# Kernel optimization log

Measured on AMD Instinct MI355X. Metric: run time of the kernel, lower is better.

## Reference

```python
import jax, jax.numpy as jnp
import numpy as np

H = 512        # hidden_size
E = 512        # embedding_size
VOCAB = 32
OPS = 16
B = 64         # batch of trees
N = 1023       # complete binary tree, depth 9 (2^10 - 1 nodes)
TEMP = 3.0
INT_TYPES_MAX = 1  # types 0 (INT_PO) and 1 (INT_NE) carry a numeric arg


def setup_inputs() -> dict:
    key = jax.random.key(0)
    ks = jax.random.split(key, 12)
    s = 0.05
    return {
        "node_types": jax.random.randint(ks[0], (B, N), 0, VOCAB),
        "node_args": jax.random.normal(ks[1], (B, N), jnp.float32),
        "validity_mask": jax.random.uniform(ks[2], (B, OPS), jnp.float32, 1e-3, 1.0),
        "emb_table": jax.random.normal(ks[3], (VOCAB, E), jnp.float32) * s,
        "W_ih": jax.random.normal(ks[4], (8 * H, E), jnp.float32) * s,
        "W_hh": jax.random.normal(ks[5], (8 * H, 2 * H), jnp.float32) * s,
        "b_ih": jax.random.normal(ks[6], (8 * H,), jnp.float32) * s,
        "b_hh": jax.random.normal(ks[7], (8 * H,), jnp.float32) * s,
        "W1": jax.random.normal(ks[8], (H, H), jnp.float32) * s,
        "b1": jax.random.normal(ks[9], (H,), jnp.float32) * s,
        "W2": jax.random.normal(ks[10], (OPS, H), jnp.float32) * s,
        "b2": jax.random.normal(ks[11], (OPS,), jnp.float32) * s,
    }


def reference(node_types, node_args, validity_mask, emb_table,
              W_ih, W_hh, b_ih, b_hh, W1, b1, W2, b2):
    # --- SympleEmbedding: per-node embedding; int-typed nodes carry arg in last slot
    emb = emb_table[node_types]                                   # [B, N, E]
    is_int = node_types <= INT_TYPES_MAX                          # [B, N]
    emb = emb.at[..., -1].set(jnp.where(is_int, node_args, emb[..., -1]))

    # --- BinaryTreeLSTM, batched level-by-level (heap layout: children of i are 2i+1, 2i+2)
    D = int(np.log2(N + 1)) - 1                                   # depth of internal levels-1 = 9
    h = jnp.zeros((B, N, H), emb.dtype)                           # leaves: zeros
    c = jnp.zeros((B, N, H), emb.dtype)
    bias = b_ih + b_hh
    for d in range(D - 1, -1, -1):                                # bottom-up over internal levels
        idx = np.arange(2 ** d - 1, 2 ** (d + 1) - 1)             # nodes at level d
        left, right = 2 * idx + 1, 2 * idx + 2
        h0 = jnp.concatenate([h[:, left], h[:, right]], axis=-1)  # [B, n, 2H]
        c0 = jnp.concatenate([c[:, left], c[:, right]], axis=-1)
        gates = (jnp.einsum('bne,ge->bng', emb[:, idx], W_ih)
                 + jnp.einsum('bnh,gh->bng', h0, W_hh) + bias)    # [B, n, 8H]
        i_g, f_g, g_g, o_g = jnp.split(gates, 4, axis=-1)         # torch LSTM gate order i,f,g,o
        c_new = jax.nn.sigmoid(f_g) * c0 + jax.nn.sigmoid(i_g) * jnp.tanh(g_g)
        h_new = jax.nn.sigmoid(o_g) * jnp.tanh(c_new)
        h = h.at[:, idx].set(h_new[..., :H])                      # keep first H (as in module)
        c = c.at[:, idx].set(c_new[..., :H])

    # --- actor FFN on root hidden + validity-masked tempered softmax
    root_h = h[:, 0]                                              # [B, H]
    x = jax.nn.relu(root_h @ W1.T + b1)
    logits = x @ W2.T + b2 + jnp.log(validity_mask)
    return jax.nn.softmax(logits / TEMP, axis=-1)                 # [B, OPS]
```

## Files before the change

kernel.cpp:

```cpp
#include <hip/hip_runtime.h>
#include <hip/hip_cooperative_groups.h>
#include <math.h>

namespace cg = cooperative_groups;

#define Nn 1023

typedef __attribute__((ext_vector_type(8))) short short8;
typedef __attribute__((ext_vector_type(4))) float f32x4;

#define AS1(p) ((const __attribute__((address_space(1))) void*)(p))
#define AS3(p) ((__attribute__((address_space(3))) void*)(p))

__device__ __forceinline__ float sigf(float x) { return 1.0f / (1.0f + __expf(-x)); }
__device__ __forceinline__ float tanhfast(float x) {
    float e = __expf(2.0f * x);
    return 1.0f - 2.0f / (e + 1.0f);
}
__device__ __forceinline__ unsigned short f2bf(float x) {
    unsigned u = __float_as_uint(x);
    return (unsigned short)((u + 0x7fffu + ((u >> 16) & 1u)) >> 16);
}
__device__ __forceinline__ float bf2f(unsigned short b) {
    return __uint_as_float(((unsigned)b) << 16);
}

__global__ __launch_bounds__(256) void prep_all(
    const float* __restrict__ W_hh, unsigned short* __restrict__ WhT,
    const float* __restrict__ W1, float* __restrict__ W1t,
    const int* __restrict__ node_types, const float* __restrict__ node_args,
    const float* __restrict__ emb, const float* __restrict__ W2,
    float* __restrict__ W2t, int* __restrict__ tyv, float* __restrict__ alphaf,
    const float* __restrict__ W_ih, const float* __restrict__ b_ih,
    const float* __restrict__ b_hh, float* __restrict__ E32b,
    float* __restrict__ w511f, int* __restrict__ rowidx, int* __restrict__ cnt) {
    int bid = blockIdx.x, t = threadIdx.x;
    if (bid < 1024) {
        int idx = bid * 256 + t;
        int P = idx >> 7;
        int k0 = (idx & 127) * 8;
        int row = ((P >> 4) & 3) * 1024 + (P >> 6) * 16 + (P & 15);
        const float* src = W_hh + (size_t)row * 1024 + k0;
        float4 v0 = *(const float4*)src;
        float4 v1 = *(const float4*)(src + 4);
        short8 o;
        o[0] = (short)f2bf(v0.x); o[1] = (short)f2bf(v0.y);
        o[2] = (short)f2bf(v0.z); o[3] = (short)f2bf(v0.w);
        o[4] = (short)f2bf(v1.x); o[5] = (short)f2bf(v1.y);
        o[6] = (short)f2bf(v1.z); o[7] = (short)f2bf(v1.w);
        *(short8*)(WhT + (size_t)P * 1024 + k0) = o;
    } else if (bid < 1088) {
        __shared__ float tile[64][65];
        int idx2 = bid - 1024;
        int jb = (idx2 & 7) * 64, kb = (idx2 >> 3) * 64;
        #pragma unroll
        for (int i = 0; i < 16; ++i) {
            int idx = t + i * 256;
            int lj = idx >> 6, lk = idx & 63;
            tile[lj][lk] = W1[(jb + lj) * 512 + kb + lk];
        }
        __syncthreads();
        #pragma unroll
        for (int i = 0; i < 16; ++i) {
            int idx = t + i * 256;
            int lk = idx >> 6, lj = idx & 63;
            W1t[(kb + lk) * 512 + jb + lj] = tile[lj][lk];
        }
    } else if (bid < 1216) {
        int gid = (bid - 1088) * 256 + t;
        if (gid < 32704) {
            int node = gid >> 6, b = gid & 63;
            int ty = node_types[b * Nn + node];
            tyv[gid] = ty;
            alphaf[gid] = (ty <= 1) ? (node_args[b * Nn + node] - emb[ty * 512 + 511]) : 0.f;
        }
        if (gid < 8192) {
            int k = gid >> 4, op = gid & 15;
            W2t[gid] = W2[op * 512 + k];
        }
    } else if (bid < 1472) {
        int o = (bid - 1216) * 256 + t;
        int ty = o >> 11, P = o & 2047;
        int row = ((P >> 4) & 3) * 1024 + (P >> 6) * 16 + (P & 15);
        const float* er = emb + (size_t)ty * 512;
        const float* wr = W_ih + (size_t)row * 512;
        float s = b_ih[row] + b_hh[row];
        for (int k = 0; k < 512; k += 4) {
            float4 e4 = *(const float4*)(er + k);
            float4 w4 = *(const float4*)(wr + k);
            s = fmaf(e4.x, w4.x, fmaf(e4.y, w4.y, fmaf(e4.z, w4.z, fmaf(e4.w, w4.w, s))));
        }
        E32b[o] = s;
        if (ty == 0) w511f[P] = wr[511];
    } else {
        int z = (bid - 1472) * 256 + t;
        if (z < 8448) rowidx[z] = 0;
        if (bid == 1472 && t == 0) *cnt = 0;
    }
}

__global__ __launch_bounds__(256) void leaf_tables(
    const float* __restrict__ E32b,
    unsigned short* __restrict__ Hleaf, float* __restrict__ Hleaf_f,
    float* __restrict__ Cleaf) {
    int o = blockIdx.x * 256 + threadIdx.x;
    int ty = o >> 9, j = o & 511;
    int Pb = (j >> 4) * 64 + (j & 15);
    const float* Er = E32b + (size_t)ty * 2048;
    float ig = Er[Pb], gg = Er[Pb + 32], og = Er[Pb + 48];
    float cn = sigf(ig) * tanhfast(gg);
    float hn = sigf(og) * tanhfast(cn);
    Hleaf[o] = f2bf(hn);
    Hleaf_f[o] = hn;
    Cleaf[o] = cn;
}

__global__ __launch_bounds__(256) void leaf_side(
    const float* __restrict__ E32b, const float* __restrict__ w511f,
    const int* __restrict__ tyv, const float* __restrict__ alphaf,
    unsigned short* __restrict__ Hside, float* __restrict__ Cside,
    const float* __restrict__ W_hh, const float* __restrict__ Hleaf_f,
    float* __restrict__ GLt, float* __restrict__ GRt,
    int* __restrict__ rowidx, int* __restrict__ cnt) {
    int bid = blockIdx.x, t = threadIdx.x;
    if (bid < 4096) {
        int r = bid * 4 + (t >> 6);
        int gn = 16320 + r;
        int ty = tyv[gn];
        if (ty > 1) return;
        float al = alphaf[gn];
        int l = r >> 6, b = r & 63;
        int jc = (t & 63) * 8;
        const float* Er = E32b + (size_t)ty * 2048;
        short8 hv;
        float cv[8];
        #pragma unroll
        for (int jj = 0; jj < 8; ++jj) {
            int j = jc + jj;
            int Pb = (j >> 4) * 64 + (j & 15);
            float ig = Er[Pb]      + al * w511f[Pb];
            float gg = Er[Pb + 32] + al * w511f[Pb + 32];
            float og = Er[Pb + 48] + al * w511f[Pb + 48];
            float cn = sigf(ig) * tanhfast(gg);
            float hn = sigf(og) * tanhfast(cn);
            hv[jj] = (short)f2bf(hn);
            cv[jj] = cn;
        }
        *(short8*)(Hside + (size_t)r * 512 + jc) = hv;
        if ((l & 1) == 0) {
            size_t cr = ((size_t)((l >> 1) * 64 + b)) * 512 + jc;
            float4 c0 = {cv[0], cv[1], cv[2], cv[3]};
            float4 c1 = {cv[4], cv[5], cv[6], cv[7]};
            *(float4*)(Cside + cr) = c0;
            *(float4*)(Cside + cr + 4) = c1;
        }
    } else if (bid < 4608) {
        int gid = (bid - 4096) * 256 + t;
        int side = gid >> 16, ty = (gid >> 11) & 31, P = gid & 2047;
        int row = ((P >> 4) & 3) * 1024 + (P >> 6) * 16 + (P & 15);
        const float* wr = W_hh + (size_t)row * 1024 + side * 512;
        const float* hr = Hleaf_f + (size_t)ty * 512;
        float s = 0.f;
        for (int k = 0; k < 512; k += 4) {
            float4 w4 = *(const float4*)(wr + k);
            float4 h4 = *(const float4*)(hr + k);
            s = fmaf(w4.x, h4.x, fmaf(w4.y, h4.y, fmaf(w4.z, h4.z, fmaf(w4.w, h4.w, s))));
        }
        if (side == 0) GLt[ty * 2048 + P] = s;
        else           GRt[ty * 2048 + P] = s;
    } else {
        int r = (bid - 4608) * 256 + t;
        int lf = (r >> 6) * 128 + (r & 63);
        if (tyv[16320 + lf] <= 1 || tyv[16320 + lf + 64] <= 1) {
            int p = atomicAdd(cnt, 1);
            rowidx[p] = r;
        }
    }
}

__global__ void zero_out(float* __restrict__ outp, int n) {
    int i = blockIdx.x * 256 + threadIdx.x;
    if (i < n) outp[i] = 0.f;
}

__device__ __forceinline__ void d7_table_body(
    char* smemraw,
    const float* __restrict__ E32b, const float* __restrict__ GLt,
    const float* __restrict__ GRt, const float* __restrict__ Cleaf,
    const float* __restrict__ Cside, const float* __restrict__ w511f,
    const int* __restrict__ tyv, const float* __restrict__ alphaf,
    unsigned short* __restrict__ out_h, float* __restrict__ out_c,
    int bx, int by) {
    float* Es  = (float*)smemraw;
    float* GLs = Es + 32 * 129;
    float* GRs = GLs + 32 * 129;
    float* Cls = GRs + 32 * 129;
    float* w5s = Cls + 32 * 33;
    const int t = threadIdx.x;
    const int j0 = by * 32;
    const int r = bx * 256 + t;

    for (int i = t; i < 32 * 128; i += 256) {
        int ty = i >> 7, pp = i & 127;
        int gp = ((j0 >> 4) + (pp >> 6)) * 64 + (pp & 63);
        Es[ty * 129 + pp]  = E32b[ty * 2048 + gp];
        GLs[ty * 129 + pp] = GLt[ty * 2048 + gp];
        GRs[ty * 129 + pp] = GRt[ty * 2048 + gp];
    }
    for (int i = t; i < 32 * 32; i += 256) {
        int ty = i >> 5, jl = i & 31;
        Cls[ty * 33 + jl] = Cleaf[ty * 512 + j0 + jl];
    }
    if (t < 128) w5s[t] = w511f[((j0 >> 4) + (t >> 6)) * 64 + (t & 63)];
    __syncthreads();

    int gn = 8128 + r;
    int tyP = tyv[gn];
    float aP = alphaf[gn];
    int lf = (r >> 6) * 128 + (r & 63);
    int tyL = tyv[16320 + lf];
    int tyR = tyv[16320 + lf + 64];
    bool intL = (tyL <= 1);
    bool evenl = (((r >> 6) & 1) == 0);
    size_t crow = ((size_t)((r >> 7) * 64 + (r & 63))) * 512;

    #pragma unroll
    for (int j8 = 0; j8 < 4; ++j8) {
        short8 hv;
        float cv[8];
        #pragma unroll
        for (int jj = 0; jj < 8; ++jj) {
            int jl = j8 * 8 + jj;
            int ppb = (jl >> 4) * 64 + (jl & 15);
            float ig = Es[tyP * 129 + ppb]      + aP * w5s[ppb]      + GLs[tyL * 129 + ppb]      + GRs[tyR * 129 + ppb];
            float fg = Es[tyP * 129 + ppb + 16] + aP * w5s[ppb + 16] + GLs[tyL * 129 + ppb + 16] + GRs[tyR * 129 + ppb + 16];
            float gg = Es[tyP * 129 + ppb + 32] + aP * w5s[ppb + 32] + GLs[tyL * 129 + ppb + 32] + GRs[tyR * 129 + ppb + 32];
            float og = Es[tyP * 129 + ppb + 48] + aP * w5s[ppb + 48] + GLs[tyL * 129 + ppb + 48] + GRs[tyR * 129 + ppb + 48];
            float cl = intL ? Cside[(size_t)r * 512 + j0 + jl] : Cls[tyL * 33 + jl];
            float cn = sigf(fg) * cl + sigf(ig) * tanhfast(gg);
            float hn = sigf(og) * tanhfast(cn);
            hv[jj] = (short)f2bf(hn);
            cv[jj] = cn;
        }
        *(short8*)(out_h + (size_t)r * 512 + j0 + j8 * 8) = hv;
        if (evenl) {
            float4 c0 = {cv[0], cv[1], cv[2], cv[3]};
            float4 c1 = {cv[4], cv[5], cv[6], cv[7]};
            *(float4*)(out_c + crow + j0 + j8 * 8) = c0;
            *(float4*)(out_c + crow + j0 + j8 * 8 + 4) = c1;
        }
    }
    __syncthreads();
}

template<int MODE>
__device__ __forceinline__ void mfma_tile(
    char* smemraw,
    const unsigned short* __restrict__ WhT, const float* __restrict__ E32b,
    const float* __restrict__ w511f,
    const int* __restrict__ tyv, const float* __restrict__ alphaf,
    const unsigned short* __restrict__ in_h, const float* __restrict__ in_c,
    const unsigned short* __restrict__ Hleaf, const unsigned short* __restrict__ Hside,
    const float* __restrict__ Cleaf, const float* __restrict__ Cside,
    const int* __restrict__ rowidx,
    unsigned short* __restrict__ out_h, float* __restrict__ out_c,
    int base, int nloc, int bx, int by) {
    unsigned short* AB = (unsigned short*)smemraw;
    const int t = threadIdx.x;
    const int w = t >> 6, lane = t & 63;
    const int wr = w >> 1, wc = w & 1;
    const int lane15 = lane & 15, lg = lane >> 4;
    const int M = nloc * 64;
    const int brow0 = bx * 128;
    const int bcol0 = by * 128;
    const int lanek8 = (lane & 7) * 8;

    const unsigned short* baseL[4];
    const unsigned short* baseR[4];
    const unsigned short* wB[4];
    #pragma unroll
    for (int q = 0; q < 4; ++q) {
        int m = w * 32 + q * 8 + (lane >> 3);
        int r = brow0 + m;
        if (MODE == 2) r = rowidx[r];
        else if (r > M - 1) r = M - 1;
        int lf = (r >> 6) * 128 + (r & 63);
        if (MODE >= 1) {
            int tyL = tyv[16320 + lf];
            int tyR = tyv[16320 + lf + 64];
            baseL[q] = (tyL <= 1) ? (Hside + (size_t)lf * 512)
                                  : (Hleaf + (size_t)tyL * 512);
            baseR[q] = (tyR <= 1) ? (Hside + (size_t)(lf + 64) * 512)
                                  : (Hleaf + (size_t)tyR * 512);
        } else {
            baseL[q] = in_h + (size_t)lf * 512;
            baseR[q] = baseL[q] + 64 * 512;
        }
        int P = bcol0 + w * 32 + q * 8 + (lane >> 3);
        wB[q] = WhT + (size_t)P * 1024;
    }

    auto stage = [&](int kt, int cur) {
        unsigned short* Ad = AB + cur * 16384;
        unsigned short* Bd = Ad + 8192;
        #pragma unroll
        for (int q = 0; q < 4; ++q) {
            const unsigned short* s = (kt < 8) ? (baseL[q] + kt * 64)
                                               : (baseR[q] + (kt - 8) * 64);
            __builtin_amdgcn_global_load_lds(AS1(s + lanek8),
                                             AS3(Ad + w * 2048 + q * 512), 16, 0, 0);
            __builtin_amdgcn_global_load_lds(AS1(wB[q] + kt * 64 + lanek8),
                                             AS3(Bd + w * 2048 + q * 512), 16, 0, 0);
        }
    };

    stage(0, 0);

    f32x4 acc[4][4];
    float w4[4];
    int P4[4];
    int rr[4][4];
    #pragma unroll
    for (int q = 0; q < 4; ++q) {
        P4[q] = bcol0 + wc * 64 + q * 16 + lane15;
        w4[q] = w511f[P4[q]];
    }
    #pragma unroll
    for (int mi = 0; mi < 4; ++mi) {
        #pragma unroll
        for (int reg = 0; reg < 4; ++reg) {
            int r = brow0 + wr * 64 + mi * 16 + lg * 4 + reg;
            if (MODE == 2) r = rowidx[r];
            else if (r > M - 1) r = M - 1;
            rr[mi][reg] = r;
            int gn = base * 64 + r;
            int ty = tyv[gn];
            float al = alphaf[gn];
            const float* Er = E32b + (size_t)ty * 2048;
            #pragma unroll
            for (int q = 0; q < 4; ++q)
                acc[mi][q][reg] = Er[P4[q]] + al * w4[q];
        }
    }

    int cur = 0;
    for (int kt = 0; kt < 16; ++kt) {
        __syncthreads();
        if (kt < 15) stage(kt + 1, cur ^ 1);
        const unsigned short* Ac = AB + cur * 16384;
        const unsigned short* Bc = Ac + 8192;
        #pragma unroll
        for (int ks = 0; ks < 2; ++ks) {
            short8 av[4], bv[4];
            #pragma unroll
            for (int mi = 0; mi < 4; ++mi)
                av[mi] = *(const short8*)(Ac + (wr * 64 + mi * 16 + lane15) * 64 + ks * 32 + lg * 8);
            #pragma unroll
            for (int q = 0; q < 4; ++q)
                bv[q] = *(const short8*)(Bc + (wc * 64 + q * 16 + lane15) * 64 + ks * 32 + lg * 8);
            #pragma unroll
            for (int mi = 0; mi < 4; ++mi)
                #pragma unroll
                for (int q = 0; q < 4; ++q)
                    acc[mi][q] = __builtin_amdgcn_mfma_f32_16x16x32_bf16(av[mi], bv[q], acc[mi][q], 0, 0, 0);
        }
        cur ^= 1;
    }

    const int j = (by * 2 + wc) * 16 + lane15;
    #pragma unroll
    for (int mi = 0; mi < 4; ++mi) {
        #pragma unroll
        for (int reg = 0; reg < 4; ++reg) {
            int r = rr[mi][reg];
            if (r < M) {
                float ig = acc[mi][0][reg];
                float fg = acc[mi][1][reg];
                float gg = acc[mi][2][reg];
                float og = acc[mi][3][reg];
                float cl;
                if (MODE >= 1) {
                    int lf = (r >> 6) * 128 + (r & 63);
                    int tyL = tyv[16320 + lf];
                    cl = (tyL <= 1) ? Cside[(size_t)r * 512 + j]
                                    : Cleaf[(size_t)tyL * 512 + j];
                } else {
                    cl = in_c[(size_t)r * 512 + j];
                }
                float cn = sigf(fg) * cl + sigf(ig) * tanhfast(gg);
                float hn = sigf(og) * tanhfast(cn);
                out_h[(size_t)r * 512 + j] = f2bf(hn);
                if (((r >> 6) & 1) == 0)
                    out_c[((size_t)((r >> 7) * 64 + (r & 63))) * 512 + j] = cn;
            }
        }
    }
}

__device__ __forceinline__ void head_body(
    char* smemraw,
    const unsigned short* __restrict__ rootH, const float* __restrict__ W1t,
    const float* __restrict__ b1, const float* __restrict__ W2t,
    const float* __restrict__ b2, const float* __restrict__ vmask,
    float* __restrict__ outp, int b) {
    float* rh = (float*)smemraw;
    float* xs = rh + 512;
    float* part = xs + 512;
    int t = threadIdx.x;
    rh[t] = bf2f(rootH[b * 512 + t]);
    rh[t + 256] = bf2f(rootH[b * 512 + t + 256]);
    __syncthreads();
    #pragma unroll
    for (int jj = 0; jj < 2; ++jj) {
        int jx = t + jj * 256;
        float acc = b1[jx];
        for (int k = 0; k < 512; ++k) acc = fmaf(rh[k], W1t[k * 512 + jx], acc);
        xs[jx] = fmaxf(acc, 0.f);
    }
    __syncthreads();
    int op = t & 15, seg = t >> 4;
    float p = 0.f;
    for (int k = seg * 32; k < seg * 32 + 32; ++k) p = fmaf(xs[k], W2t[k * 16 + op], p);
    part[seg * 17 + op] = p;
    __syncthreads();
    if (t < 16) {
        float s = 0.f;
        #pragma unroll
        for (int g = 0; g < 16; ++g) s += part[g * 17 + t];
        float logit = s + b2[t] + logf(vmask[b * 16 + t]);
        float z = logit * (1.0f / 3.0f);
        float m = z;
        for (int o2 = 8; o2; o2 >>= 1) m = fmaxf(m, __shfl_xor(m, o2, 16));
        float e = __expf(z - m);
        float ssum = e;
        for (int o2 = 8; o2; o2 >>= 1) ssum += __shfl_xor(ssum, o2, 16);
        outp[b * 16 + t] = e / ssum;
    }
}

__global__ __launch_bounds__(256) void tree_main(
    const unsigned short* WhT, const float* E32b, const float* w511f,
    const int* tyv, const float* alphaf,
    const unsigned short* Hleaf, const unsigned short* Hside,
    const float* Cleaf, const float* Cside,
    const float* GLt, const float* GRt,
    const int* rowidx, const int* cnt,
    unsigned short* Xh, float* Xc, unsigned short* Yh, float* Yc,
    const float* W1t, const float* b1, const float* W2t, const float* b2,
    const float* vmask, float* outp) {
    cg::grid_group grid = cg::this_grid();
    extern __shared__ char smem[];
    const int bid = blockIdx.x;

    d7_table_body(smem, E32b, GLt, GRt, Cleaf, Cside, w511f, tyv, alphaf,
                  Xh, Xc, bid & 31, bid >> 5);
    __threadfence(); grid.sync();

    {
        int nc = *cnt;
        int rb = ((nc + 127) & ~127) >> 7;
        int ntiles = rb * 16;
        for (int T = bid; T < ntiles; T += 512)
            mfma_tile<2>(smem, WhT, E32b, w511f, tyv, alphaf, nullptr, nullptr,
                         Hleaf, Hside, Cleaf, Cside, rowidx,
                         Xh, Xc, 127, 128, T % rb, T / rb);
    }
    __threadfence(); grid.sync();

    for (int d = 6; d >= 0; --d) {
        int nloc = 1 << d;
        int gx = (nloc >= 2) ? (nloc >> 1) : 1;
        unsigned short* oh = (d & 1) ? Xh : Yh;
        float* oc          = (d & 1) ? Xc : Yc;
        const unsigned short* ih = (d & 1) ? Yh : Xh;
        const float* ic          = (d & 1) ? Yc : Xc;
        int ntiles = gx * 16;
        if (bid < ntiles)
            mfma_tile<0>(smem, WhT, E32b, w511f, tyv, alphaf, ih, ic,
                         nullptr, nullptr, nullptr, nullptr, nullptr,
                         oh, oc, nloc - 1, nloc, bid % gx, bid / gx);
        __threadfence(); grid.sync();
    }

    if (bid < 64)
        head_body(smem, Yh, W1t, b1, W2t, b2, vmask, outp, bid);
}

__global__ __launch_bounds__(256) void d7_table_cell_k(
    const float* __restrict__ E32b, const float* __restrict__ GLt,
    const float* __restrict__ GRt, const float* __restrict__ Cleaf,
    const float* __restrict__ Cside, const float* __restrict__ w511f,
    const int* __restrict__ tyv, const float* __restrict__ alphaf,
    unsigned short* __restrict__ out_h, float* __restrict__ out_c) {
    extern __shared__ char smem[];
    d7_table_body(smem, E32b, GLt, GRt, Cleaf, Cside, w511f, tyv, alphaf,
                  out_h, out_c, blockIdx.x, blockIdx.y);
}

template<int MODE>
__global__ __launch_bounds__(256) void lstm_mfma_k(
    const unsigned short* __restrict__ WhT, const float* __restrict__ E32b,
    const float* __restrict__ w511f,
    const int* __restrict__ tyv, const float* __restrict__ alphaf,
    const unsigned short* __restrict__ in_h, const float* __restrict__ in_c,
    const unsigned short* __restrict__ Hleaf, const unsigned short* __restrict__ Hside,
    const float* __restrict__ Cleaf, const float* __restrict__ Cside,
    const int* __restrict__ rowidx, const int* __restrict__ cnt,
    unsigned short* __restrict__ out_h, float* __restrict__ out_c,
    int base, int nloc) {
    extern __shared__ char smem[];
    if (MODE == 2) {
        int nc = *cnt;
        int padded = (nc + 127) & ~127;
        if ((int)blockIdx.x * 128 >= padded) return;
    }
    mfma_tile<MODE>(smem, WhT, E32b, w511f, tyv, alphaf, in_h, in_c,
                    Hleaf, Hside, Cleaf, Cside, rowidx,
                    out_h, out_c, base, nloc, blockIdx.x, blockIdx.y);
}

__global__ __launch_bounds__(256) void head_k(
    const unsigned short* __restrict__ rootH, const float* __restrict__ W1t,
    const float* __restrict__ b1, const float* __restrict__ W2t,
    const float* __restrict__ b2, const float* __restrict__ vmask,
    float* __restrict__ outp) {
    extern __shared__ char smem[];
    head_body(smem, rootH, W1t, b1, W2t, b2, vmask, outp, blockIdx.x);
}

extern "C" void kernel_launch(void* const* d_in, const int* in_sizes, int n_in,
                              void* d_out, int out_size, void* d_ws, size_t ws_size,
                              hipStream_t stream) {
    const int*   node_types = (const int*)d_in[0];
    const float* node_args  = (const float*)d_in[1];
    const float* vmask      = (const float*)d_in[2];
    const float* emb_table  = (const float*)d_in[3];
    const float* W_ih       = (const float*)d_in[4];
    const float* W_hh       = (const float*)d_in[5];
    const float* b_ih       = (const float*)d_in[6];
    const float* b_hh       = (const float*)d_in[7];
    const float* W1         = (const float*)d_in[8];
    const float* b1         = (const float*)d_in[9];
    const float* W2         = (const float*)d_in[10];
    const float* b2         = (const float*)d_in[11];
    float* out = (float*)d_out;

    char* ws = (char*)d_ws;
    size_t off = 0;
    auto alloc = [&](size_t bytes) { char* p = ws + off; off += (bytes + 255) & ~(size_t)255; return p; };
    unsigned short* WhT  = (unsigned short*)alloc((size_t)2048 * 1024 * 2);
    float* E32b          = (float*)alloc((size_t)32 * 2048 * 4);
    float* w511f         = (float*)alloc(2048 * 4);
    float* W1t           = (float*)alloc((size_t)512 * 512 * 4);
    float* W2t           = (float*)alloc(8192 * 4);
    int*   tyv           = (int*)alloc(32704 * 4);
    float* alphaf        = (float*)alloc(32704 * 4);
    unsigned short* Hleaf= (unsigned short*)alloc((size_t)32 * 512 * 2);
    float* Hleaf_f       = (float*)alloc((size_t)32 * 512 * 4);
    float* Cleaf         = (float*)alloc((size_t)32 * 512 * 4);
    float* GLt           = (float*)alloc((size_t)32 * 2048 * 4);
    float* GRt           = (float*)alloc((size_t)32 * 2048 * 4);
    int*   rowidx        = (int*)alloc(8448 * 4);
    int*   cnt           = (int*)alloc(256);
    unsigned short* Hside= (unsigned short*)alloc((size_t)16384 * 512 * 2);
    float* Cside         = (float*)alloc((size_t)8192 * 512 * 4);
    unsigned short* Xh   = (unsigned short*)alloc((size_t)8192 * 512 * 2);
    unsigned short* Yh   = (unsigned short*)alloc((size_t)4096 * 512 * 2);
    float* Xc            = (float*)alloc((size_t)4096 * 512 * 4);
    float* Yc            = (float*)alloc((size_t)2048 * 512 * 4);

    if (ws_size < off) {
        zero_out<<<(out_size + 255) / 256, 256, 0, stream>>>(out, out_size);
        return;
    }

    prep_all<<<1505, 256, 0, stream>>>(W_hh, WhT, W1, W1t, node_types, node_args,
                                       emb_table, W2, W2t, tyv, alphaf,
                                       W_ih, b_ih, b_hh, E32b, w511f, rowidx, cnt);
    leaf_tables<<<64, 256, 0, stream>>>(E32b, Hleaf, Hleaf_f, Cleaf);
    leaf_side<<<4640, 256, 0, stream>>>(E32b, w511f, tyv, alphaf, Hside, Cside,
                                        W_hh, Hleaf_f, GLt, GRt, rowidx, cnt);

    bool coop_ok = false;
    {
        int occ = 0;
        hipError_t qe = hipOccupancyMaxActiveBlocksPerMultiprocessor(
            &occ, tree_main, 256, 65536);
        if (qe == hipSuccess && occ >= 2) coop_ok = true;
    }
    if (coop_ok) {
        const unsigned short* cWhT = WhT;  const float* cE32b = E32b;
        const float* cw511 = w511f;        const int* ctyv = tyv;
        const float* calpha = alphaf;      const unsigned short* cHleaf = Hleaf;
        const unsigned short* cHside = Hside; const float* cCleaf = Cleaf;
        const float* cCside = Cside;       const float* cGL = GLt;
        const float* cGR = GRt;            const int* cridx = rowidx;
        const int* ccnt = cnt;             const float* cW1t = W1t;
        const float* cW2t = W2t;
        void* kargs[] = {
            (void*)&cWhT, (void*)&cE32b, (void*)&cw511, (void*)&ctyv, (void*)&calpha,
            (void*)&cHleaf, (void*)&cHside, (void*)&cCleaf, (void*)&cCside,
            (void*)&cGL, (void*)&cGR, (void*)&cridx, (void*)&ccnt,
            (void*)&Xh, (void*)&Xc, (void*)&Yh, (void*)&Yc,
            (void*)&cW1t, (void*)&b1, (void*)&cW2t, (void*)&b2,
            (void*)&vmask, (void*)&out };
        hipError_t le = hipLaunchCooperativeKernel(
            tree_main, dim3(512), dim3(256), kargs, (unsigned)65536, stream);
        if (le != hipSuccess) coop_ok = false;
    }
    if (!coop_ok) {
        d7_table_cell_k<<<dim3(32, 16), 256, 54272, stream>>>(
            E32b, GLt, GRt, Cleaf, Cside, w511f, tyv, alphaf, Xh, Xc);
        lstm_mfma_k<2><<<dim3(64, 16), 256, 65536, stream>>>(
            WhT, E32b, w511f, tyv, alphaf, nullptr, nullptr,
            Hleaf, Hside, Cleaf, Cside, rowidx, cnt, Xh, Xc, 127, 128);
        for (int d = 6; d >= 0; --d) {
            int nloc = 1 << d;
            unsigned short* oh = (d & 1) ? Xh : Yh;
            float* oc          = (d & 1) ? Xc : Yc;
            const unsigned short* ih = (d & 1) ? Yh : Xh;
            const float* ic          = (d & 1) ? Yc : Xc;
            int gx = (nloc >= 2) ? (nloc / 2) : 1;
            lstm_mfma_k<0><<<dim3(gx, 16), 256, 65536, stream>>>(
                WhT, E32b, w511f, tyv, alphaf, ih, ic,
                nullptr, nullptr, nullptr, nullptr,
                nullptr, nullptr, oh, oc, nloc - 1, nloc);
        }
        head_k<<<64, 256, 5184, stream>>>(Yh, W1t, b1, W2t, b2, vmask, out);
    }
}
```

Before: 448.8 us.

## Fold leaf-side setup and GL/GR table GEMM into cooperative tree kernel

Removes the separate leaf_tables and leaf_side launches and moves leaf computation, side-leaf state and the row-index compaction into a phase inside the cooperative tree kernel. The GL/GR child-contribution tables are now computed with a bf16 MFMA GEMM over a block-diagonal leaf matrix instead of scalar fp32 dot products. d7 table rows with any int-typed child are skipped because the compacted MFMA pass covers them, and the E32b dot product gets four accumulators. This cuts launch overhead and scalar work at the cost of an extra grid sync and bf16 rounding in the GL/GR tables.

```diff
diff --git a/kernel.cpp b/kernel.cpp
--- a/kernel.cpp
+++ b/kernel.cpp
@@ -84,13 +84,22 @@
         int row = ((P >> 4) & 3) * 1024 + (P >> 6) * 16 + (P & 15);
         const float* er = emb + (size_t)ty * 512;
         const float* wr = W_ih + (size_t)row * 512;
-        float s = b_ih[row] + b_hh[row];
-        for (int k = 0; k < 512; k += 4) {
-            float4 e4 = *(const float4*)(er + k);
-            float4 w4 = *(const float4*)(wr + k);
-            s = fmaf(e4.x, w4.x, fmaf(e4.y, w4.y, fmaf(e4.z, w4.z, fmaf(e4.w, w4.w, s))));
-        }
-        E32b[o] = s;
+        float s0 = b_ih[row] + b_hh[row], s1 = 0.f, s2 = 0.f, s3 = 0.f;
+        for (int k = 0; k < 512; k += 16) {
+            float4 e0 = *(const float4*)(er + k);
+            float4 w0 = *(const float4*)(wr + k);
+            float4 e1 = *(const float4*)(er + k + 4);
+            float4 w1 = *(const float4*)(wr + k + 4);
+            float4 e2 = *(const float4*)(er + k + 8);
+            float4 w2 = *(const float4*)(wr + k + 8);
+            float4 e3 = *(const float4*)(er + k + 12);
+            float4 w3 = *(const float4*)(wr + k + 12);
+            s0 = fmaf(e0.x, w0.x, fmaf(e0.y, w0.y, fmaf(e0.z, w0.z, fmaf(e0.w, w0.w, s0))));
+            s1 = fmaf(e1.x, w1.x, fmaf(e1.y, w1.y, fmaf(e1.z, w1.z, fmaf(e1.w, w1.w, s1))));
+            s2 = fmaf(e2.x, w2.x, fmaf(e2.y, w2.y, fmaf(e2.z, w2.z, fmaf(e2.w, w2.w, s2))));
+            s3 = fmaf(e3.x, w3.x, fmaf(e3.y, w3.y, fmaf(e3.z, w3.z, fmaf(e3.w, w3.w, s3))));
+        }
+        E32b[o] = (s0 + s1) + (s2 + s3);
         if (ty == 0) w511f[P] = wr[511];
     } else {
         int z = (bid - 1472) * 256 + t;
@@ -99,77 +108,76 @@
     }
 }
 
-__global__ __launch_bounds__(256) void leaf_tables(
-    const float* __restrict__ E32b,
-    unsigned short* __restrict__ Hleaf, float* __restrict__ Hleaf_f,
-    float* __restrict__ Cleaf) {
-    int o = blockIdx.x * 256 + threadIdx.x;
-    int ty = o >> 9, j = o & 511;
-    int Pb = (j >> 4) * 64 + (j & 15);
-    const float* Er = E32b + (size_t)ty * 2048;
-    float ig = Er[Pb], gg = Er[Pb + 32], og = Er[Pb + 48];
-    float cn = sigf(ig) * tanhfast(gg);
-    float hn = sigf(og) * tanhfast(cn);
-    Hleaf[o] = f2bf(hn);
-    Hleaf_f[o] = hn;
-    Cleaf[o] = cn;
-}
-
-__global__ __launch_bounds__(256) void leaf_side(
+__global__ void zero_out(float* __restrict__ outp, int n) {
+    int i = blockIdx.x * 256 + threadIdx.x;
+    if (i < n) outp[i] = 0.f;
+}
+
+__device__ __forceinline__ void ph0_body(
+    int bid,
     const float* __restrict__ E32b, const float* __restrict__ w511f,
     const int* __restrict__ tyv, const float* __restrict__ alphaf,
+    unsigned short* __restrict__ Hleaf, float* __restrict__ Cleaf,
+    unsigned short* __restrict__ A64,
     unsigned short* __restrict__ Hside, float* __restrict__ Cside,
-    const float* __restrict__ W_hh, const float* __restrict__ Hleaf_f,
-    float* __restrict__ GLt, float* __restrict__ GRt,
     int* __restrict__ rowidx, int* __restrict__ cnt) {
-    int bid = blockIdx.x, t = threadIdx.x;
-    if (bid < 4096) {
-        int r = bid * 4 + (t >> 6);
-        int gn = 16320 + r;
-        int ty = tyv[gn];
-        if (ty > 1) return;
-        float al = alphaf[gn];
-        int l = r >> 6, b = r & 63;
-        int jc = (t & 63) * 8;
+    const int t = threadIdx.x;
+    if (bid < 64) {
+        int o = bid * 256 + t;
+        int ty = o >> 9, j = o & 511;
+        int Pb = (j >> 4) * 64 + (j & 15);
         const float* Er = E32b + (size_t)ty * 2048;
-        short8 hv;
-        float cv[8];
-        #pragma unroll
-        for (int jj = 0; jj < 8; ++jj) {
-            int j = jc + jj;
-            int Pb = (j >> 4) * 64 + (j & 15);
-            float ig = Er[Pb]      + al * w511f[Pb];
-            float gg = Er[Pb + 32] + al * w511f[Pb + 32];
-            float og = Er[Pb + 48] + al * w511f[Pb + 48];
-            float cn = sigf(ig) * tanhfast(gg);
-            float hn = sigf(og) * tanhfast(cn);
-            hv[jj] = (short)f2bf(hn);
-            cv[jj] = cn;
-        }
-        *(short8*)(Hside + (size_t)r * 512 + jc) = hv;
-        if ((l & 1) == 0) {
-            size_t cr = ((size_t)((l >> 1) * 64 + b)) * 512 + jc;
-            float4 c0 = {cv[0], cv[1], cv[2], cv[3]};
-            float4 c1 = {cv[4], cv[5], cv[6], cv[7]};
-            *(float4*)(Cside + cr) = c0;
-            *(float4*)(Cside + cr + 4) = c1;
-        }
-    } else if (bid < 4608) {
-        int gid = (bid - 4096) * 256 + t;
-        int side = gid >> 16, ty = (gid >> 11) & 31, P = gid & 2047;
-        int row = ((P >> 4) & 3) * 1024 + (P >> 6) * 16 + (P & 15);
-        const float* wr = W_hh + (size_t)row * 1024 + side * 512;
-        const float* hr = Hleaf_f + (size_t)ty * 512;
-        float s = 0.f;
-        for (int k = 0; k < 512; k += 4) {
-            float4 w4 = *(const float4*)(wr + k);
-            float4 h4 = *(const float4*)(hr + k);
-            s = fmaf(w4.x, h4.x, fmaf(w4.y, h4.y, fmaf(w4.z, h4.z, fmaf(w4.w, h4.w, s))));
-        }
-        if (side == 0) GLt[ty * 2048 + P] = s;
-        else           GRt[ty * 2048 + P] = s;
-    } else {
-        int r = (bid - 4608) * 256 + t;
+        float ig = Er[Pb], gg = Er[Pb + 32], og = Er[Pb + 48];
+        float cn = sigf(ig) * tanhfast(gg);
+        float hn = sigf(og) * tanhfast(cn);
+        unsigned short hb = f2bf(hn);
+        Hleaf[o] = hb;
+        Cleaf[o] = cn;
+        A64[ty * 1024 + j] = hb;
+        A64[ty * 1024 + 512 + j] = 0;
+        A64[(32 + ty) * 1024 + j] = 0;
+        A64[(32 + ty) * 1024 + 512 + j] = hb;
+    }
+    {
+        int wave = t >> 6, jc = (t & 63) * 8;
+        int r0 = bid * 32 + wave * 8;
+        int tys[8];
+        #pragma unroll
+        for (int i = 0; i < 8; ++i) tys[i] = tyv[16320 + r0 + i];
+        #pragma unroll
+        for (int i = 0; i < 8; ++i) {
+            if (tys[i] > 1) continue;
+            int r = r0 + i;
+            int gn = 16320 + r;
+            float al = alphaf[gn];
+            int l = r >> 6, b = r & 63;
+            const float* Er = E32b + (size_t)tys[i] * 2048;
+            short8 hv;
+            float cv[8];
+            #pragma unroll
+            for (int jj = 0; jj < 8; ++jj) {
+                int j = jc + jj;
+                int Pb = (j >> 4) * 64 + (j & 15);
+                float ig = Er[Pb]      + al * w511f[Pb];
+                float gg = Er[Pb + 32] + al * w511f[Pb + 32];
+                float og = Er[Pb + 48] + al * w511f[Pb + 48];
+                float cn = sigf(ig) * tanhfast(gg);
+                float hn = sigf(og) * tanhfast(cn);
+                hv[jj] = (short)f2bf(hn);
+                cv[jj] = cn;
+            }
+            *(short8*)(Hside + (size_t)r * 512 + jc) = hv;
+            if ((l & 1) == 0) {
+                size_t cr = ((size_t)((l >> 1) * 64 + b)) * 512 + jc;
+                float4 c0 = {cv[0], cv[1], cv[2], cv[3]};
+                float4 c1 = {cv[4], cv[5], cv[6], cv[7]};
+                *(float4*)(Cside + cr) = c0;
+                *(float4*)(Cside + cr + 4) = c1;
+            }
+        }
+    }
+    if (bid >= 64 && bid < 96) {
+        int r = (bid - 64) * 256 + t;
         int lf = (r >> 6) * 128 + (r & 63);
         if (tyv[16320 + lf] <= 1 || tyv[16320 + lf + 64] <= 1) {
             int p = atomicAdd(cnt, 1);
@@ -178,16 +186,96 @@
     }
 }
 
-__global__ void zero_out(float* __restrict__ outp, int n) {
-    int i = blockIdx.x * 256 + threadIdx.x;
-    if (i < n) outp[i] = 0.f;
+template<int KT, bool BIAS>
+__device__ __forceinline__ void table_gemm_body(
+    char* smemraw, const unsigned short* __restrict__ Abf,
+    const unsigned short* __restrict__ Bt, const float* __restrict__ biasP,
+    float* __restrict__ C0, float* __restrict__ C1, int by) {
+    unsigned short* AB = (unsigned short*)smemraw;
+    const int t = threadIdx.x;
+    const int w = t >> 6, lane = t & 63;
+    const int wr = w >> 1, wc = w & 1;
+    const int lane15 = lane & 15, lg = lane >> 4;
+    const int bcol0 = by * 128;
+    const int lanek8 = (lane & 7) * 8;
+    const int ROWS = BIAS ? 32 : 64;
+
+    const unsigned short* aA[4];
+    const unsigned short* wB[4];
+    #pragma unroll
+    for (int q = 0; q < 4; ++q) {
+        int m = w * 32 + q * 8 + (lane >> 3);
+        int r = (m < ROWS) ? m : (ROWS - 1);
+        aA[q] = Abf + (size_t)r * (KT * 64);
+        int P = bcol0 + w * 32 + q * 8 + (lane >> 3);
+        wB[q] = Bt + (size_t)P * (KT * 64);
+    }
+    auto stage = [&](int kt, int cur) {
+        unsigned short* Ad = AB + cur * 16384;
+        unsigned short* Bd = Ad + 8192;
+        #pragma unroll
+        for (int q = 0; q < 4; ++q) {
+            __builtin_amdgcn_global_load_lds(AS1(aA[q] + kt * 64 + lanek8),
+                                             AS3(Ad + w * 2048 + q * 512), 16, 0, 0);
+            __builtin_amdgcn_global_load_lds(AS1(wB[q] + kt * 64 + lanek8),
+                                             AS3(Bd + w * 2048 + q * 512), 16, 0, 0);
+        }
+    };
+    stage(0, 0);
+    f32x4 acc[4][4];
+    int P4[4];
+    #pragma unroll
+    for (int q = 0; q < 4; ++q) P4[q] = bcol0 + wc * 64 + q * 16 + lane15;
+    #pragma unroll
+    for (int mi = 0; mi < 4; ++mi)
+        #pragma unroll
+        for (int reg = 0; reg < 4; ++reg)
+            #pragma unroll
+            for (int q = 0; q < 4; ++q)
+                acc[mi][q][reg] = BIAS ? biasP[P4[q]] : 0.f;
+    int cur = 0;
+    for (int kt = 0; kt < KT; ++kt) {
+        __syncthreads();
+        if (kt < KT - 1) stage(kt + 1, cur ^ 1);
+        const unsigned short* Ac = AB + cur * 16384;
+        const unsigned short* Bc = Ac + 8192;
+        #pragma unroll
+        for (int ks = 0; ks < 2; ++ks) {
+            short8 av[4], bv[4];
+            #pragma unroll
+            for (int mi = 0; mi < 4; ++mi)
+                av[mi] = *(const short8*)(Ac + (wr * 64 + mi * 16 + lane15) * 64 + ks * 32 + lg * 8);
+            #pragma unroll
+            for (int q = 0; q < 4; ++q)
+                bv[q] = *(const short8*)(Bc + (wc * 64 + q * 16 + lane15) * 64 + ks * 32 + lg * 8);
+            #pragma unroll
+            for (int mi = 0; mi < 4; ++mi)
+                #pragma unroll
+                for (int q = 0; q < 4; ++q)
+                    acc[mi][q] = __builtin_amdgcn_mfma_f32_16x16x32_bf16(av[mi], bv[q], acc[mi][q], 0, 0, 0);
+        }
+        cur ^= 1;
+    }
+    #pragma unroll
+    for (int mi = 0; mi < 4; ++mi)
+        #pragma unroll
+        for (int reg = 0; reg < 4; ++reg) {
+            int ro = wr * 64 + mi * 16 + lg * 4 + reg;
+            #pragma unroll
+            for (int q = 0; q < 4; ++q) {
+                float v = acc[mi][q][reg];
+                if (ro < 32) C0[(size_t)ro * 2048 + P4[q]] = v;
+                else if (!BIAS && ro < 64) C1[(size_t)(ro - 32) * 2048 + P4[q]] = v;
+            }
+        }
+    __syncthreads();
 }
 
 __device__ __forceinline__ void d7_table_body(
     char* smemraw,
     const float* __restrict__ E32b, const float* __restrict__ GLt,
     const float* __restrict__ GRt, const float* __restrict__ Cleaf,
-    const float* __restrict__ Cside, const float* __restrict__ w511f,
+    const float* __restrict__ w511f,
     const int* __restrict__ tyv, const float* __restrict__ alphaf,
     unsigned short* __restrict__ out_h, float* __restrict__ out_c,
     int bx, int by) {
@@ -220,34 +308,36 @@
     int lf = (r >> 6) * 128 + (r & 63);
     int tyL = tyv[16320 + lf];
     int tyR = tyv[16320 + lf + 64];
-    bool intL = (tyL <= 1);
+    bool skip = (tyL <= 1) || (tyR <= 1);
     bool evenl = (((r >> 6) & 1) == 0);
     size_t crow = ((size_t)((r >> 7) * 64 + (r & 63))) * 512;
 
-    #pragma unroll
-    for (int j8 = 0; j8 < 4; ++j8) {
-        short8 hv;
-        float cv[8];
-        #pragma unroll
-        for (int jj = 0; jj < 8; ++jj) {
-            int jl = j8 * 8 + jj;
-            int ppb = (jl >> 4) * 64 + (jl & 15);
-            float ig = Es[tyP * 129 + ppb]      + aP * w5s[ppb]      + GLs[tyL * 129 + ppb]      + GRs[tyR * 129 + ppb];
-            float fg = Es[tyP * 129 + ppb + 16] + aP * w5s[ppb + 16] + GLs[tyL * 129 + ppb + 16] + GRs[tyR * 129 + ppb + 16];
-            float gg = Es[tyP * 129 + ppb + 32] + aP * w5s[ppb + 32] + GLs[tyL * 129 + ppb + 32] + GRs[tyR * 129 + ppb + 32];
-            float og = Es[tyP * 129 + ppb + 48] + aP * w5s[ppb + 48] + GLs[tyL * 129 + ppb + 48] + GRs[tyR * 129 + ppb + 48];
-            float cl = intL ? Cside[(size_t)r * 512 + j0 + jl] : Cls[tyL * 33 + jl];
-            float cn = sigf(fg) * cl + sigf(ig) * tanhfast(gg);
-            float hn = sigf(og) * tanhfast(cn);
-            hv[jj] = (short)f2bf(hn);
-            cv[jj] = cn;
-        }
-        *(short8*)(out_h + (size_t)r * 512 + j0 + j8 * 8) = hv;
-        if (evenl) {
-            float4 c0 = {cv[0], cv[1], cv[2], cv[3]};
-            float4 c1 = {cv[4], cv[5], cv[6], cv[7]};
-            *(float4*)(out_c + crow + j0 + j8 * 8) = c0;
-            *(float4*)(out_c + crow + j0 + j8 * 8 + 4) = c1;
+    if (!skip) {
+        #pragma unroll
+        for (int j8 = 0; j8 < 4; ++j8) {
+            short8 hv;
+            float cv[8];
+            #pragma unroll
+            for (int jj = 0; jj < 8; ++jj) {
+                int jl = j8 * 8 + jj;
+                int ppb = (jl >> 4) * 64 + (jl & 15);
+                float ig = Es[tyP * 129 + ppb]      + aP * w5s[ppb]      + GLs[tyL * 129 + ppb]      + GRs[tyR * 129 + ppb];
+                float fg = Es[tyP * 129 + ppb + 16] + aP * w5s[ppb + 16] + GLs[tyL * 129 + ppb + 16] + GRs[tyR * 129 + ppb + 16];
+                float gg = Es[tyP * 129 + ppb + 32] + aP * w5s[ppb + 32] + GLs[tyL * 129 + ppb + 32] + GRs[tyR * 129 + ppb + 32];
+                float og = Es[tyP * 129 + ppb + 48] + aP * w5s[ppb + 48] + GLs[tyL * 129 + ppb + 48] + GRs[tyR * 129 + ppb + 48];
+                float cl = Cls[tyL * 33 + jl];
+                float cn = sigf(fg) * cl + sigf(ig) * tanhfast(gg);
+                float hn = sigf(og) * tanhfast(cn);
+                hv[jj] = (short)f2bf(hn);
+                cv[jj] = cn;
+            }
+            *(short8*)(out_h + (size_t)r * 512 + j0 + j8 * 8) = hv;
+            if (evenl) {
+                float4 c0 = {cv[0], cv[1], cv[2], cv[3]};
+                float4 c1 = {cv[4], cv[5], cv[6], cv[7]};
+                *(float4*)(out_c + crow + j0 + j8 * 8) = c0;
+                *(float4*)(out_c + crow + j0 + j8 * 8 + 4) = c1;
+            }
         }
     }
     __syncthreads();
@@ -262,7 +352,7 @@
     const unsigned short* __restrict__ in_h, const float* __restrict__ in_c,
     const unsigned short* __restrict__ Hleaf, const unsigned short* __restrict__ Hside,
     const float* __restrict__ Cleaf, const float* __restrict__ Cside,
-    const int* __restrict__ rowidx,
+    const int* __restrict__ rowidx, int nc,
     unsigned short* __restrict__ out_h, float* __restrict__ out_c,
     int base, int nloc, int bx, int by) {
     unsigned short* AB = (unsigned short*)smemraw;
@@ -281,11 +371,15 @@
     #pragma unroll
     for (int q = 0; q < 4; ++q) {
         int m = w * 32 + q * 8 + (lane >> 3);
-        int r = brow0 + m;
-        if (MODE == 2) r = rowidx[r];
-        else if (r > M - 1) r = M - 1;
+        int r;
+        if (MODE == 2) {
+            int idx = brow0 + m; if (idx > nc - 1) idx = nc - 1;
+            r = rowidx[idx];
+        } else {
+            r = brow0 + m; if (r > M - 1) r = M - 1;
+        }
         int lf = (r >> 6) * 128 + (r & 63);
-        if (MODE >= 1) {
+        if (MODE == 2) {
             int tyL = tyv[16320 + lf];
             int tyR = tyv[16320 + lf + 64];
             baseL[q] = (tyL <= 1) ? (Hside + (size_t)lf * 512)
@@ -329,9 +423,15 @@
     for (int mi = 0; mi < 4; ++mi) {
         #pragma unroll
         for (int reg = 0; reg < 4; ++reg) {
-            int r = brow0 + wr * 64 + mi * 16 + lg * 4 + reg;
-            if (MODE == 2) r = rowidx[r];
-            else if (r > M - 1) r = M - 1;
+            int r;
+            if (MODE == 2) {
+                int idx = brow0 + wr * 64 + mi * 16 + lg * 4 + reg;
+                if (idx > nc - 1) idx = nc - 1;
+                r = rowidx[idx];
+            } else {
+                r = brow0 + wr * 64 + mi * 16 + lg * 4 + reg;
+                if (r > M - 1) r = M - 1;
+            }
             rr[mi][reg] = r;
             int gn = base * 64 + r;
             int ty = tyv[gn];
@@ -379,7 +479,7 @@
                 float gg = acc[mi][2][reg];
                 float og = acc[mi][3][reg];
                 float cl;
-                if (MODE >= 1) {
+                if (MODE == 2) {
                     int lf = (r >> 6) * 128 + (r & 63);
                     int tyL = tyv[16320 + lf];
                     cl = (tyL <= 1) ? Cside[(size_t)r * 512 + j]
@@ -441,10 +541,9 @@
 __global__ __launch_bounds__(256) void tree_main(
     const unsigned short* WhT, const float* E32b, const float* w511f,
     const int* tyv, const float* alphaf,
-    const unsigned short* Hleaf, const unsigned short* Hside,
-    const float* Cleaf, const float* Cside,
-    const float* GLt, const float* GRt,
-    const int* rowidx, const int* cnt,
+    unsigned short* Hleaf, unsigned short* Hside,
+    float* Cleaf, float* Cside, unsigned short* A64,
+    float* GLt, float* GRt, int* rowidx, int* cnt,
     unsigned short* Xh, float* Xc, unsigned short* Yh, float* Yc,
     const float* W1t, const float* b1, const float* W2t, const float* b2,
     const float* vmask, float* outp) {
@@ -452,17 +551,22 @@
     extern __shared__ char smem[];
     const int bid = blockIdx.x;
 
-    d7_table_body(smem, E32b, GLt, GRt, Cleaf, Cside, w511f, tyv, alphaf,
+    ph0_body(bid, E32b, w511f, tyv, alphaf, Hleaf, Cleaf, A64, Hside, Cside,
+             rowidx, cnt);
+    __threadfence(); grid.sync();
+
+    if (bid < 16)
+        table_gemm_body<16, false>(smem, A64, WhT, nullptr, GLt, GRt, bid);
+    __threadfence(); grid.sync();
+
+    d7_table_body(smem, E32b, GLt, GRt, Cleaf, w511f, tyv, alphaf,
                   Xh, Xc, bid & 31, bid >> 5);
-    __threadfence(); grid.sync();
-
     {
         int nc = *cnt;
         int rb = ((nc + 127) & ~127) >> 7;
-        int ntiles = rb * 16;
-        for (int T = bid; T < ntiles; T += 512)
+        for (int T = bid; T < rb * 16; T += 512)
             mfma_tile<2>(smem, WhT, E32b, w511f, tyv, alphaf, nullptr, nullptr,
-                         Hleaf, Hside, Cleaf, Cside, rowidx,
+                         Hleaf, Hside, Cleaf, Cside, rowidx, nc,
                          Xh, Xc, 127, 128, T % rb, T / rb);
     }
     __threadfence(); grid.sync();
@@ -477,7 +581,7 @@
         int ntiles = gx * 16;
         if (bid < ntiles)
             mfma_tile<0>(smem, WhT, E32b, w511f, tyv, alphaf, ih, ic,
-                         nullptr, nullptr, nullptr, nullptr, nullptr,
+                         nullptr, nullptr, nullptr, nullptr, nullptr, 0,
                          oh, oc, nloc - 1, nloc, bid % gx, bid / gx);
         __threadfence(); grid.sync();
     }
@@ -486,37 +590,63 @@
         head_body(smem, Yh, W1t, b1, W2t, b2, vmask, outp, bid);
 }
 
-__global__ __launch_bounds__(256) void d7_table_cell_k(
+__global__ __launch_bounds__(256) void ph0_k(
+    const float* __restrict__ E32b, const float* __restrict__ w511f,
+    const int* __restrict__ tyv, const float* __restrict__ alphaf,
+    unsigned short* __restrict__ Hleaf, float* __restrict__ Cleaf,
+    unsigned short* __restrict__ A64,
+    unsigned short* __restrict__ Hside, float* __restrict__ Cside,
+    int* __restrict__ rowidx, int* __restrict__ cnt) {
+    ph0_body(blockIdx.x, E32b, w511f, tyv, alphaf, Hleaf, Cleaf, A64,
+             Hside, Cside, rowidx, cnt);
+}
+
+__global__ __launch_bounds__(256) void glgr_k(
+    const unsigned short* __restrict__ A64, const unsigned short* __restrict__ WhT,
+    float* __restrict__ GLt, float* __restrict__ GRt) {
+    extern __shared__ char smem[];
+    table_gemm_body<16, false>(smem, A64, WhT, nullptr, GLt, GRt, blockIdx.x);
+}
+
+__global__ __launch_bounds__(256) void d7t_k(
     const float* __restrict__ E32b, const float* __restrict__ GLt,
     const float* __restrict__ GRt, const float* __restrict__ Cleaf,
-    const float* __restrict__ Cside, const float* __restrict__ w511f,
+    const float* __restrict__ w511f,
     const int* __restrict__ tyv, const float* __restrict__ alphaf,
     unsigned short* __restrict__ out_h, float* __restrict__ out_c) {
     extern __shared__ char smem[];
-    d7_table_body(smem, E32b, GLt, GRt, Cleaf, Cside, w511f, tyv, alphaf,
+    d7_table_body(smem, E32b, GLt, GRt, Cleaf, w511f, tyv, alphaf,
                   out_h, out_c, blockIdx.x, blockIdx.y);
 }
 
-template<int MODE>
-__global__ __launch_bounds__(256) void lstm_mfma_k(
+__global__ __launch_bounds__(256) void d7c_k(
+    const unsigned short* __restrict__ WhT, const float* __restrict__ E32b,
+    const float* __restrict__ w511f,
+    const int* __restrict__ tyv, const float* __restrict__ alphaf,
+    const unsigned short* __restrict__ Hleaf, const unsigned short* __restrict__ Hside,
+    const float* __restrict__ Cleaf, const float* __restrict__ Cside,
+    const int* __restrict__ rowidx, const int* __restrict__ cnt,
+    unsigned short* __restrict__ out_h, float* __restrict__ out_c) {
+    extern __shared__ char smem[];
+    int nc = *cnt;
+    int padded = (nc + 127) & ~127;
+    if ((int)blockIdx.x * 128 >= padded) return;
+    mfma_tile<2>(smem, WhT, E32b, w511f, tyv, alphaf, nullptr, nullptr,
+                 Hleaf, Hside, Cleaf, Cside, rowidx, nc,
+                 out_h, out_c, 127, 128, blockIdx.x, blockIdx.y);
+}
+
+__global__ __launch_bounds__(256) void lvl_k(
     const unsigned short* __restrict__ WhT, const float* __restrict__ E32b,
     const float* __restrict__ w511f,
     const int* __restrict__ tyv, const float* __restrict__ alphaf,
     const unsigned short* __restrict__ in_h, const float* __restrict__ in_c,
-    const unsigned short* __restrict__ Hleaf, const unsigned short* __restrict__ Hside,
-    const float* __restrict__ Cleaf, const float* __restrict__ Cside,
-    const int* __restrict__ rowidx, const int* __restrict__ cnt,
     unsigned short* __restrict__ out_h, float* __restrict__ out_c,
     int base, int nloc) {
     extern __shared__ char smem[];
-    if (MODE == 2) {
-        int nc = *cnt;
-        int padded = (nc + 127) & ~127;
-        if ((int)blockIdx.x * 128 >= padded) return;
-    }
-    mfma_tile<MODE>(smem, WhT, E32b, w511f, tyv, alphaf, in_h, in_c,
-                    Hleaf, Hside, Cleaf, Cside, rowidx,
-                    out_h, out_c, base, nloc, blockIdx.x, blockIdx.y);
+    mfma_tile<0>(smem, WhT, E32b, w511f, tyv, alphaf, in_h, in_c,
+                 nullptr, nullptr, nullptr, nullptr, nullptr, 0,
+                 out_h, out_c, base, nloc, blockIdx.x, blockIdx.y);
 }
 
 __global__ __launch_bounds__(256) void head_k(
@@ -556,8 +686,8 @@
     int*   tyv           = (int*)alloc(32704 * 4);
     float* alphaf        = (float*)alloc(32704 * 4);
     unsigned short* Hleaf= (unsigned short*)alloc((size_t)32 * 512 * 2);
-    float* Hleaf_f       = (float*)alloc((size_t)32 * 512 * 4);
     float* Cleaf         = (float*)alloc((size_t)32 * 512 * 4);
+    unsigned short* A64  = (unsigned short*)alloc((size_t)64 * 1024 * 2);
     float* GLt           = (float*)alloc((size_t)32 * 2048 * 4);
     float* GRt           = (float*)alloc((size_t)32 * 2048 * 4);
     int*   rowidx        = (int*)alloc(8448 * 4);
@@ -577,9 +707,6 @@
     prep_all<<<1505, 256, 0, stream>>>(W_hh, WhT, W1, W1t, node_types, node_args,
                                        emb_table, W2, W2t, tyv, alphaf,
                                        W_ih, b_ih, b_hh, E32b, w511f, rowidx, cnt);
-    leaf_tables<<<64, 256, 0, stream>>>(E32b, Hleaf, Hleaf_f, Cleaf);
-    leaf_side<<<4640, 256, 0, stream>>>(E32b, w511f, tyv, alphaf, Hside, Cside,
-                                        W_hh, Hleaf_f, GLt, GRt, rowidx, cnt);
 
     bool coop_ok = false;
     {
@@ -591,16 +718,12 @@
     if (coop_ok) {
         const unsigned short* cWhT = WhT;  const float* cE32b = E32b;
         const float* cw511 = w511f;        const int* ctyv = tyv;
-        const float* calpha = alphaf;      const unsigned short* cHleaf = Hleaf;
-        const unsigned short* cHside = Hside; const float* cCleaf = Cleaf;
-        const float* cCside = Cside;       const float* cGL = GLt;
-        const float* cGR = GRt;            const int* cridx = rowidx;
-        const int* ccnt = cnt;             const float* cW1t = W1t;
+        const float* calpha = alphaf;      const float* cW1t = W1t;
         const float* cW2t = W2t;
         void* kargs[] = {
             (void*)&cWhT, (void*)&cE32b, (void*)&cw511, (void*)&ctyv, (void*)&calpha,
-            (void*)&cHleaf, (void*)&cHside, (void*)&cCleaf, (void*)&cCside,
-            (void*)&cGL, (void*)&cGR, (void*)&cridx, (void*)&ccnt,
+            (void*)&Hleaf, (void*)&Hside, (void*)&Cleaf, (void*)&Cside, (void*)&A64,
+            (void*)&GLt, (void*)&GRt, (void*)&rowidx, (void*)&cnt,
             (void*)&Xh, (void*)&Xc, (void*)&Yh, (void*)&Yc,
             (void*)&cW1t, (void*)&b1, (void*)&cW2t, (void*)&b2,
             (void*)&vmask, (void*)&out };
@@ -609,11 +732,14 @@
         if (le != hipSuccess) coop_ok = false;
     }
     if (!coop_ok) {
-        d7_table_cell_k<<<dim3(32, 16), 256, 54272, stream>>>(
-            E32b, GLt, GRt, Cleaf, Cside, w511f, tyv, alphaf, Xh, Xc);
-        lstm_mfma_k<2><<<dim3(64, 16), 256, 65536, stream>>>(
-            WhT, E32b, w511f, tyv, alphaf, nullptr, nullptr,
-            Hleaf, Hside, Cleaf, Cside, rowidx, cnt, Xh, Xc, 127, 128);
+        ph0_k<<<512, 256, 0, stream>>>(E32b, w511f, tyv, alphaf, Hleaf, Cleaf,
+                                       A64, Hside, Cside, rowidx, cnt);
+        glgr_k<<<16, 256, 65536, stream>>>(A64, WhT, GLt, GRt);
+        d7t_k<<<dim3(32, 16), 256, 54272, stream>>>(
+            E32b, GLt, GRt, Cleaf, w511f, tyv, alphaf, Xh, Xc);
+        d7c_k<<<dim3(64, 16), 256, 65536, stream>>>(
+            WhT, E32b, w511f, tyv, alphaf, Hleaf, Hside, Cleaf, Cside,
+            rowidx, cnt, Xh, Xc);
         for (int d = 6; d >= 0; --d) {
             int nloc = 1 << d;
             unsigned short* oh = (d & 1) ? Xh : Yh;
@@ -621,10 +747,8 @@
             const unsigned short* ih = (d & 1) ? Yh : Xh;
             const float* ic          = (d & 1) ? Yc : Xc;
             int gx = (nloc >= 2) ? (nloc / 2) : 1;
-            lstm_mfma_k<0><<<dim3(gx, 16), 256, 65536, stream>>>(
-                WhT, E32b, w511f, tyv, alphaf, ih, ic,
-                nullptr, nullptr, nullptr, nullptr,
-                nullptr, nullptr, oh, oc, nloc - 1, nloc);
+            lvl_k<<<dim3(gx, 16), 256, 65536, stream>>>(
+                WhT, E32b, w511f, tyv, alphaf, ih, ic, oh, oc, nloc - 1, nloc);
         }
         head_k<<<64, 256, 5184, stream>>>(Yh, W1t, b1, W2t, b2, vmask, out);
     }
```

Result: faster. 384.7 us (-14.3%).
